# Performance work log

Measured on AMD Instinct MI355X. Metric: run time of the kernel, lower is better.

## Reference

```python
import jax, jax.numpy as jnp
import numpy as np

E, C, O = 500_000, 64, 64

def setup_inputs() -> dict:
    key = jax.random.key(0)
    k1, k2, k3, k4 = jax.random.split(key, 4)
    x = jax.random.normal(k1, (E, C), dtype=jnp.float32)
    # neighbors in [-1, E): -1 marks a missing neighbor (boundary edge)
    neighbors = jax.random.randint(k2, (E, 4), -1, E, dtype=jnp.int32)
    # Linear(5C -> O): kaiming-ish init
    W = jax.random.normal(k3, (O, 5 * C), dtype=jnp.float32) * (1.0 / np.sqrt(5 * C))
    b = jax.random.normal(k4, (O,), dtype=jnp.float32) * 0.01
    return {"x": x, "neighbors": neighbors, "W": W, "b": b}

def reference(x, neighbors, W, b):
    E_, C_ = x.shape
    safe_nb = jnp.maximum(neighbors, 0)                      # clamp(min=0)
    nb_feats = x[safe_nb]                                    # [E, 4, C] gather
    missing = (neighbors < 0)[..., None]                     # [E, 4, 1]
    nb_feats = jnp.where(missing, jnp.zeros((), x.dtype), nb_feats)
    pair1 = jnp.sort(nb_feats[:, 0:2, :], axis=1)            # elementwise sort of 2
    pair2 = jnp.sort(nb_feats[:, 2:4, :], axis=1)
    combined = jnp.concatenate(
        [x, pair1.reshape(E_, 2 * C_), pair2.reshape(E_, 2 * C_)], axis=1
    )                                                         # [E, 5C]
    return combined @ W.T + b                                 # [E, O]
```

## Files before the change

### kernel.cpp

```cpp
#include <hip/hip_runtime.h>

#define E_TOT 500000
#define C_DIM 64
#define K_DIM 320

typedef __attribute__((ext_vector_type(8))) short bf16x8;
typedef __attribute__((ext_vector_type(4))) float f32x4;

__device__ __forceinline__ short f2bf(float f) {
  unsigned u = __float_as_uint(f);
  unsigned r = u + 0x7fffu + ((u >> 16) & 1u);
  return (short)(r >> 16);
}
__device__ __forceinline__ float bf2f(short s) {
  return __uint_as_float(((unsigned)(unsigned short)s) << 16);
}

__global__ __launch_bounds__(512, 2)
void meshconv_kernel(const float* __restrict__ x, const int* __restrict__ nbr,
                     const float* __restrict__ W, const float* __restrict__ bias,
                     float* __restrict__ out) {
  __shared__ short Whf[20480];
  __shared__ short Wlf[20480];

  const int tid = threadIdx.x;

  for (int fidx = tid; fidx < 2560; fidx += 512) {
    const int l   = fidx & 63;
    const int t   = (fidx >> 6) & 3;
    const int ks  = fidx >> 8;
    const int row = t * 16 + (l & 15);
    const int col = ks * 32 + (l >> 4) * 8;
    const float* src = W + row * K_DIM + col;
    float4 u = *(const float4*)(src);
    float4 v = *(const float4*)(src + 4);
    float f[8] = {u.x, u.y, u.z, u.w, v.x, v.y, v.z, v.w};
    bf16x8 hv, lv;
#pragma unroll
    for (int j = 0; j < 8; ++j) {
      short h = f2bf(f[j]);
      hv[j] = h;
      lv[j] = f2bf(f[j] - bf2f(h));
    }
    *reinterpret_cast<bf16x8*>(&Whf[fidx * 8]) = hv;
    *reinterpret_cast<bf16x8*>(&Wlf[fidx * 8]) = lv;
  }
  __syncthreads();

  const int lane = tid & 63;
  const int wv   = tid >> 6;
  const int lrow = lane & 15;
  const int kc   = (lane >> 4) * 8;

  const int base = blockIdx.x * 256 + wv * 32;
  const int e0  = base + lrow;
  const int e1  = base + 16 + lrow;
  const int ec0 = min(e0, E_TOT - 1);
  const int ec1 = min(e1, E_TOT - 1);

  const int4 nb0 = *(const int4*)(nbr + ec0 * 4);
  const int4 nb1 = *(const int4*)(nbr + ec1 * 4);

  f32x4 acc[2][4];
#pragma unroll
  for (int m = 0; m < 2; ++m)
#pragma unroll
    for (int t = 0; t < 4; ++t) acc[m][t] = (f32x4){0.f, 0.f, 0.f, 0.f};

  auto load8 = [&](int row, int h, float* f) {
    const float* p = x + row * C_DIM + h * 32 + kc;
    float4 u = *(const float4*)(p);
    float4 v = *(const float4*)(p + 4);
    f[0] = u.x; f[1] = u.y; f[2] = u.z; f[3] = u.w;
    f[4] = v.x; f[5] = v.y; f[6] = v.z; f[7] = v.w;
  };
  auto cvt = [&](const float* f, bf16x8& hv, bf16x8& lv) {
#pragma unroll
    for (int j = 0; j < 8; ++j) {
      short h = f2bf(f[j]);
      hv[j] = h;
      lv[j] = f2bf(f[j] - bf2f(h));
    }
  };
  auto dot_step = [&](int ks, bf16x8 ah0, bf16x8 al0, bf16x8 ah1, bf16x8 al1) {
#pragma unroll
    for (int t = 0; t < 4; ++t) {
      const int off = ((ks * 4 + t) * 64 + lane) * 8;
      bf16x8 wh = *reinterpret_cast<const bf16x8*>(&Whf[off]);
      bf16x8 wl = *reinterpret_cast<const bf16x8*>(&Wlf[off]);
      acc[0][t] = __builtin_amdgcn_mfma_f32_16x16x32_bf16(ah0, wh, acc[0][t], 0, 0, 0);
      acc[0][t] = __builtin_amdgcn_mfma_f32_16x16x32_bf16(ah0, wl, acc[0][t], 0, 0, 0);
      acc[0][t] = __builtin_amdgcn_mfma_f32_16x16x32_bf16(al0, wh, acc[0][t], 0, 0, 0);
      acc[1][t] = __builtin_amdgcn_mfma_f32_16x16x32_bf16(ah1, wh, acc[1][t], 0, 0, 0);
      acc[1][t] = __builtin_amdgcn_mfma_f32_16x16x32_bf16(ah1, wl, acc[1][t], 0, 0, 0);
      acc[1][t] = __builtin_amdgcn_mfma_f32_16x16x32_bf16(al1, wh, acc[1][t], 0, 0, 0);
    }
  };

#pragma unroll
  for (int h = 0; h < 2; ++h) {
    float f0[8], f1[8];
    load8(ec0, h, f0);
    load8(ec1, h, f1);
    bf16x8 ah0, al0, ah1, al1;
    cvt(f0, ah0, al0);
    cvt(f1, ah1, al1);
    dot_step(h, ah0, al0, ah1, al1);
  }

#pragma unroll
  for (int p = 0; p < 2; ++p) {
    const int nA0 = p ? nb0.z : nb0.x;
    const int nB0 = p ? nb0.w : nb0.y;
    const int nA1 = p ? nb1.z : nb1.x;
    const int nB1 = p ? nb1.w : nb1.y;
#pragma unroll
    for (int h = 0; h < 2; ++h) {
      float fa0[8], fb0[8], fa1[8], fb1[8];
      load8(max(nA0, 0), h, fa0);
      load8(max(nB0, 0), h, fb0);
      load8(max(nA1, 0), h, fa1);
      load8(max(nB1, 0), h, fb1);
      float mn0[8], mx0[8], mn1[8], mx1[8];
#pragma unroll
      for (int j = 0; j < 8; ++j) {
        float a0  = (nA0 < 0) ? 0.f : fa0[j];
        float b0v = (nB0 < 0) ? 0.f : fb0[j];
        float a1  = (nA1 < 0) ? 0.f : fa1[j];
        float b1v = (nB1 < 0) ? 0.f : fb1[j];
        mn0[j] = fminf(a0, b0v);  mx0[j] = fmaxf(a0, b0v);
        mn1[j] = fminf(a1, b1v);  mx1[j] = fmaxf(a1, b1v);
      }
      bf16x8 mnh0, mnl0, mxh0, mxl0, mnh1, mnl1, mxh1, mxl1;
      cvt(mn0, mnh0, mnl0);  cvt(mx0, mxh0, mxl0);
      cvt(mn1, mnh1, mnl1);  cvt(mx1, mxh1, mxl1);
      dot_step(2 + 4 * p + h, mnh0, mnl0, mnh1, mnl1);
      dot_step(4 + 4 * p + h, mxh0, mxl0, mxh1, mxl1);
    }
  }

  float bv[4];
#pragma unroll
  for (int t = 0; t < 4; ++t) bv[t] = bias[t * 16 + lrow];

  const int lgrp = lane >> 4;
#pragma unroll
  for (int m = 0; m < 2; ++m)
#pragma unroll
    for (int r = 0; r < 4; ++r) {
      const int e = base + m * 16 + lgrp * 4 + r;
      if (e < E_TOT) {
        float* po = out + e * 64 + lrow;
        po[0]  = acc[m][0][r] + bv[0];
        po[16] = acc[m][1][r] + bv[1];
        po[32] = acc[m][2][r] + bv[2];
        po[48] = acc[m][3][r] + bv[3];
      }
    }
}

extern "C" void kernel_launch(void* const* d_in, const int* in_sizes, int n_in,
                              void* d_out, int out_size, void* d_ws, size_t ws_size,
                              hipStream_t stream) {
  const float* x   = (const float*)d_in[0];
  const int*   nbr = (const int*)d_in[1];
  const float* W   = (const float*)d_in[2];
  const float* b   = (const float*)d_in[3];
  float* out = (float*)d_out;
  const int blocks = (E_TOT + 255) / 256;
  hipLaunchKernelGGL(meshconv_kernel, dim3(blocks), dim3(512), 0, stream,
                     x, nbr, W, b, out);
}
```

Measured before the change: 314.8 us.

## Switch split-precision MFMA from bf16 to fp16 and double block size

Replaces the manual bf16 hi/lo split with hardware fp16 conversions and fp16 MFMA instructions, which removes the integer rounding arithmetic in every conversion. The block grows from 512 to 1024 threads, each covering 512 edges, so the weight matrix is staged into shared memory half as many times in total. The risk is fp16 range overflow or underflow for large or tiny values, and fewer resident blocks per CU with a different register budget under launch_bounds(1024).

Result: faster. 300.7 us (-4.5%).

```diff
diff --git a/kernel.cpp b/kernel.cpp
--- a/kernel.cpp
+++ b/kernel.cpp
@@ -4,28 +4,19 @@
 #define C_DIM 64
 #define K_DIM 320
 
-typedef __attribute__((ext_vector_type(8))) short bf16x8;
+typedef __attribute__((ext_vector_type(8))) _Float16 half8;
 typedef __attribute__((ext_vector_type(4))) float f32x4;
 
-__device__ __forceinline__ short f2bf(float f) {
-  unsigned u = __float_as_uint(f);
-  unsigned r = u + 0x7fffu + ((u >> 16) & 1u);
-  return (short)(r >> 16);
-}
-__device__ __forceinline__ float bf2f(short s) {
-  return __uint_as_float(((unsigned)(unsigned short)s) << 16);
-}
-
-__global__ __launch_bounds__(512, 2)
+__global__ __launch_bounds__(1024)
 void meshconv_kernel(const float* __restrict__ x, const int* __restrict__ nbr,
                      const float* __restrict__ W, const float* __restrict__ bias,
                      float* __restrict__ out) {
-  __shared__ short Whf[20480];
-  __shared__ short Wlf[20480];
+  __shared__ _Float16 Whf[20480];
+  __shared__ _Float16 Wlf[20480];
 
   const int tid = threadIdx.x;
 
-  for (int fidx = tid; fidx < 2560; fidx += 512) {
+  for (int fidx = tid; fidx < 2560; fidx += 1024) {
     const int l   = fidx & 63;
     const int t   = (fidx >> 6) & 3;
     const int ks  = fidx >> 8;
@@ -35,15 +26,15 @@
     float4 u = *(const float4*)(src);
     float4 v = *(const float4*)(src + 4);
     float f[8] = {u.x, u.y, u.z, u.w, v.x, v.y, v.z, v.w};
-    bf16x8 hv, lv;
+    half8 hv, lv;
 #pragma unroll
     for (int j = 0; j < 8; ++j) {
-      short h = f2bf(f[j]);
+      _Float16 h = (_Float16)f[j];
       hv[j] = h;
-      lv[j] = f2bf(f[j] - bf2f(h));
+      lv[j] = (_Float16)(f[j] - (float)h);
     }
-    *reinterpret_cast<bf16x8*>(&Whf[fidx * 8]) = hv;
-    *reinterpret_cast<bf16x8*>(&Wlf[fidx * 8]) = lv;
+    *reinterpret_cast<half8*>(&Whf[fidx * 8]) = hv;
+    *reinterpret_cast<half8*>(&Wlf[fidx * 8]) = lv;
   }
   __syncthreads();
 
@@ -52,7 +43,7 @@
   const int lrow = lane & 15;
   const int kc   = (lane >> 4) * 8;
 
-  const int base = blockIdx.x * 256 + wv * 32;
+  const int base = blockIdx.x * 512 + wv * 32;
   const int e0  = base + lrow;
   const int e1  = base + 16 + lrow;
   const int ec0 = min(e0, E_TOT - 1);
@@ -74,26 +65,26 @@
     f[0] = u.x; f[1] = u.y; f[2] = u.z; f[3] = u.w;
     f[4] = v.x; f[5] = v.y; f[6] = v.z; f[7] = v.w;
   };
-  auto cvt = [&](const float* f, bf16x8& hv, bf16x8& lv) {
+  auto cvt = [&](const float* f, half8& hv, half8& lv) {
 #pragma unroll
     for (int j = 0; j < 8; ++j) {
-      short h = f2bf(f[j]);
+      _Float16 h = (_Float16)f[j];
       hv[j] = h;
-      lv[j] = f2bf(f[j] - bf2f(h));
+      lv[j] = (_Float16)(f[j] - (float)h);
     }
   };
-  auto dot_step = [&](int ks, bf16x8 ah0, bf16x8 al0, bf16x8 ah1, bf16x8 al1) {
+  auto dot_step = [&](int ks, half8 ah0, half8 al0, half8 ah1, half8 al1) {
 #pragma unroll
     for (int t = 0; t < 4; ++t) {
       const int off = ((ks * 4 + t) * 64 + lane) * 8;
-      bf16x8 wh = *reinterpret_cast<const bf16x8*>(&Whf[off]);
-      bf16x8 wl = *reinterpret_cast<const bf16x8*>(&Wlf[off]);
-      acc[0][t] = __builtin_amdgcn_mfma_f32_16x16x32_bf16(ah0, wh, acc[0][t], 0, 0, 0);
-      acc[0][t] = __builtin_amdgcn_mfma_f32_16x16x32_bf16(ah0, wl, acc[0][t], 0, 0, 0);
-      acc[0][t] = __builtin_amdgcn_mfma_f32_16x16x32_bf16(al0, wh, acc[0][t], 0, 0, 0);
-      acc[1][t] = __builtin_amdgcn_mfma_f32_16x16x32_bf16(ah1, wh, acc[1][t], 0, 0, 0);
-      acc[1][t] = __builtin_amdgcn_mfma_f32_16x16x32_bf16(ah1, wl, acc[1][t], 0, 0, 0);
-      acc[1][t] = __builtin_amdgcn_mfma_f32_16x16x32_bf16(al1, wh, acc[1][t], 0, 0, 0);
+      half8 wh = *reinterpret_cast<const half8*>(&Whf[off]);
+      half8 wl = *reinterpret_cast<const half8*>(&Wlf[off]);
+      acc[0][t] = __builtin_amdgcn_mfma_f32_16x16x32_f16(ah0, wh, acc[0][t], 0, 0, 0);
+      acc[0][t] = __builtin_amdgcn_mfma_f32_16x16x32_f16(ah0, wl, acc[0][t], 0, 0, 0);
+      acc[0][t] = __builtin_amdgcn_mfma_f32_16x16x32_f16(al0, wh, acc[0][t], 0, 0, 0);
+      acc[1][t] = __builtin_amdgcn_mfma_f32_16x16x32_f16(ah1, wh, acc[1][t], 0, 0, 0);
+      acc[1][t] = __builtin_amdgcn_mfma_f32_16x16x32_f16(ah1, wl, acc[1][t], 0, 0, 0);
+      acc[1][t] = __builtin_amdgcn_mfma_f32_16x16x32_f16(al1, wh, acc[1][t], 0, 0, 0);
     }
   };
 
@@ -102,7 +93,7 @@
     float f0[8], f1[8];
     load8(ec0, h, f0);
     load8(ec1, h, f1);
-    bf16x8 ah0, al0, ah1, al1;
+    half8 ah0, al0, ah1, al1;
     cvt(f0, ah0, al0);
     cvt(f1, ah1, al1);
     dot_step(h, ah0, al0, ah1, al1);
@@ -131,7 +122,7 @@
         mn0[j] = fminf(a0, b0v);  mx0[j] = fmaxf(a0, b0v);
         mn1[j] = fminf(a1, b1v);  mx1[j] = fmaxf(a1, b1v);
       }
-      bf16x8 mnh0, mnl0, mxh0, mxl0, mnh1, mnl1, mxh1, mxl1;
+      half8 mnh0, mnl0, mxh0, mxl0, mnh1, mnl1, mxh1, mxl1;
       cvt(mn0, mnh0, mnl0);  cvt(mx0, mxh0, mxl0);
       cvt(mn1, mnh1, mnl1);  cvt(mx1, mxh1, mxl1);
       dot_step(2 + 4 * p + h, mnh0, mnl0, mnh1, mnl1);
@@ -167,7 +158,7 @@
   const float* W   = (const float*)d_in[2];
   const float* b   = (const float*)d_in[3];
   float* out = (float*)d_out;
-  const int blocks = (E_TOT + 255) / 256;
-  hipLaunchKernelGGL(meshconv_kernel, dim3(blocks), dim3(512), 0, stream,
+  const int blocks = (E_TOT + 511) / 512;
+  hipLaunchKernelGGL(meshconv_kernel, dim3(blocks), dim3(1024), 0, stream,
                      x, nbr, W, b, out);
 }
```
